# Kernel tuning notes

Hardware: AMD Instinct MI355X
Metric: run time of the kernel (lower is better)

Reference implementation:

```python
import jax, jax.numpy as jnp
import numpy as np

FFT_LEN = 512
FFT_BINS = FFT_LEN // 2 + 1  # 257


def _dft_kernels(fft_len):
    n = np.arange(fft_len)
    k = np.arange(fft_len // 2 + 1).reshape(-1, 1)
    ang = 2.0 * np.pi * k * n / fft_len
    real_kernel = jnp.asarray(np.cos(ang), dtype=jnp.float32)   # (bins, fft_len)
    imag_kernel = jnp.asarray(-np.sin(ang), dtype=jnp.float32)  # (bins, fft_len)
    return real_kernel, imag_kernel


def setup_inputs() -> dict:
    key = jax.random.key(0)
    x = jax.random.normal(key, (16, 4000, FFT_LEN), dtype=jnp.float32)
    real_kernel, imag_kernel = _dft_kernels(FFT_LEN)
    return {"x": x, "real_kernel": real_kernel, "imag_kernel": imag_kernel}


def reference(x, real_kernel, imag_kernel):
    # x: (B, F, N); kernels: (K, N) with K = N//2 + 1
    B, F, _ = x.shape
    real = jnp.einsum("bfn,kn->bfk", x, real_kernel)  # (B, F, K)
    imag = jnp.einsum("bfn,kn->bfk", x, imag_kernel)  # (B, F, K)
    # interleave real/imag per frequency bin: [..., r0, i0, r1, i1, ...]
    out = jnp.stack([real, imag], axis=-1).reshape(B, F, -1)  # (B, F, 2K)
    return out
```

## Files before the change

### kernel.cpp

```cpp
#include <hip/hip_runtime.h>

typedef _Float16 f16x8 __attribute__((ext_vector_type(8)));
typedef float f32x4 __attribute__((ext_vector_type(4)));

#define MDIM 64000
#define KDIM 512
#define NCOLS 514
#define NPAD 640
#define BM 128
#define BN 128
#define BK 64
#define NT 5
#define NWG 2500

#define GLOAD_LDS16(g, l)                                        \
  __builtin_amdgcn_global_load_lds(                              \
      (const __attribute__((address_space(1))) void*)(g),        \
      (__attribute__((address_space(3))) void*)(l), 16, 0, 0)

__global__ void prep_w(const float* __restrict__ rk, const float* __restrict__ ik,
                       _Float16* __restrict__ wb) {
  int n = blockIdx.x;
  int k = threadIdx.x;
  float v = 0.0f;
  if (n < NCOLS) {
    int bin = n >> 1;
    const float* src = (n & 1) ? ik : rk;
    v = src[bin * KDIM + k];
  }
  wb[(size_t)n * KDIM + k] = (_Float16)v;
}

__global__ __launch_bounds__(256, 3)
void dft_gemm(const float* __restrict__ x, const _Float16* __restrict__ wb,
              float* __restrict__ out) {
  __shared__ float As[BM * BK];
  __shared__ _Float16 Bs[BN * BK];

  const int tid = threadIdx.x;
  const int l   = tid & 63;
  const int w   = tid >> 6;
  const int lr  = l & 15;
  const int lg  = l >> 4;
  const int wm  = (w >> 1) * 64;
  const int wn  = (w & 1) * 64;

  const int xcd = blockIdx.x & 7;
  const int lid = blockIdx.x >> 3;
  const int q   = NWG >> 3;
  const int r   = NWG & 7;
  const int wgid = (xcd < r) ? xcd * (q + 1) + lid
                             : r * (q + 1) + (xcd - r) * q + lid;
  const int mt = wgid / NT;
  const int nt = wgid - mt * NT;
  const int m0 = mt * BM;
  const int n0 = nt * BN;

  f32x4 acc[4][4] = {};

  const int arl = l >> 4;
  const int acp = l & 15;
  const int brl = l >> 3;
  const int bcp = l & 7;

  for (int kt = 0; kt < KDIM / BK; ++kt) {
    if (kt) __syncthreads();

#pragma unroll
    for (int s = 0; s < 8; ++s) {
      int r0  = w * 32 + s * 4;
      int row = r0 + arl;
      int cl  = acp ^ (row & 7);
      const float* g = x + (size_t)(m0 + row) * KDIM + kt * BK + cl * 4;
      GLOAD_LDS16(g, &As[r0 * BK]);
    }
#pragma unroll
    for (int s = 0; s < 4; ++s) {
      int r0  = w * 32 + s * 8;
      int row = r0 + brl;
      int cl  = bcp ^ (row & 7);
      const _Float16* g = wb + (size_t)(n0 + row) * KDIM + kt * BK + cl * 8;
      GLOAD_LDS16(g, &Bs[r0 * BK]);
    }
    __syncthreads();

#pragma unroll
    for (int ks = 0; ks < 2; ++ks) {
      f16x8 av[4], bv[4];
#pragma unroll
      for (int fm = 0; fm < 4; ++fm) {
        int row = wm + fm * 16 + lr;
        int c0  = ks * 8 + lg * 2;
        int sw  = row & 7;
        f32x4 lo = *reinterpret_cast<const f32x4*>(&As[row * BK + ((c0 ^ sw) << 2)]);
        f32x4 hi = *reinterpret_cast<const f32x4*>(&As[row * BK + (((c0 + 1) ^ sw) << 2)]);
        f16x8 h;
        h[0] = (_Float16)lo[0]; h[1] = (_Float16)lo[1];
        h[2] = (_Float16)lo[2]; h[3] = (_Float16)lo[3];
        h[4] = (_Float16)hi[0]; h[5] = (_Float16)hi[1];
        h[6] = (_Float16)hi[2]; h[7] = (_Float16)hi[3];
        av[fm] = h;
      }
#pragma unroll
      for (int fn = 0; fn < 4; ++fn) {
        int row = wn + fn * 16 + lr;
        int c   = (ks * 4 + lg) ^ (row & 7);
        bv[fn] = *reinterpret_cast<const f16x8*>(&Bs[row * BK + (c << 3)]);
      }
#pragma unroll
      for (int fm = 0; fm < 4; ++fm)
#pragma unroll
        for (int fn = 0; fn < 4; ++fn)
          acc[fm][fn] = __builtin_amdgcn_mfma_f32_16x16x32_f16(
              av[fm], bv[fn], acc[fm][fn], 0, 0, 0);
    }
  }

#pragma unroll
  for (int fm = 0; fm < 4; ++fm) {
#pragma unroll
    for (int rr = 0; rr < 4; ++rr) {
      int row = m0 + wm + fm * 16 + lg * 4 + rr;
      size_t base = (size_t)row * NCOLS;
#pragma unroll
      for (int fn = 0; fn < 4; ++fn) {
        int col = n0 + wn + fn * 16 + lr;
        if (col < NCOLS) out[base + col] = acc[fm][fn][rr];
      }
    }
  }
}

extern "C" void kernel_launch(void* const* d_in, const int* in_sizes, int n_in,
                              void* d_out, int out_size, void* d_ws, size_t ws_size,
                              hipStream_t stream) {
  const float* x  = (const float*)d_in[0];
  const float* rk = (const float*)d_in[1];
  const float* ik = (const float*)d_in[2];
  float* out = (float*)d_out;
  _Float16* wb = (_Float16*)d_ws;

  prep_w<<<dim3(NPAD), dim3(KDIM), 0, stream>>>(rk, ik, wb);

  dim3 grid(NWG);
  dft_gemm<<<grid, dim3(256), 0, stream>>>(x, wb, out);
}
```

Baseline: 81.90 us.

## Double-buffer LDS and convert A to fp16 via registers before staging

Loads of the fp32 input tile now go through registers. They are converted to fp16 once and stored into a swizzled fp16 LDS buffer, replacing the earlier direct global-to-LDS fp32 copy that was converted on every LDS read. A and B are double-buffered, so the loads for the next K tile are issued before computing on the current one, and only one barrier is needed per iteration. This trades extra VGPRs for prefetched A data (launch bounds lowered from 3 to 2 waves per SIMD) for overlap of memory and MFMA work and halved A LDS traffic.

```diff
diff --git a/kernel.cpp b/kernel.cpp
--- a/kernel.cpp
+++ b/kernel.cpp
@@ -10,6 +10,7 @@
 #define BM 128
 #define BN 128
 #define BK 64
+#define KT (KDIM / BK)
 #define NT 5
 #define NWG 2500
 
@@ -31,11 +32,11 @@
   wb[(size_t)n * KDIM + k] = (_Float16)v;
 }
 
-__global__ __launch_bounds__(256, 3)
+__global__ __launch_bounds__(256, 2)
 void dft_gemm(const float* __restrict__ x, const _Float16* __restrict__ wb,
               float* __restrict__ out) {
-  __shared__ float As[BM * BK];
-  __shared__ _Float16 Bs[BN * BK];
+  __shared__ _Float16 As[2][BM * BK];
+  __shared__ _Float16 Bs[2][BN * BK];
 
   const int tid = threadIdx.x;
   const int l   = tid & 63;
@@ -58,62 +59,93 @@
 
   f32x4 acc[4][4] = {};
 
-  const int arl = l >> 4;
-  const int acp = l & 15;
+  const int arow = tid >> 1;
+  const int acol = (tid & 1) * 32;
+  const float* aptr = x + (size_t)(m0 + arow) * KDIM + acol;
+
   const int brl = l >> 3;
   const int bcp = l & 7;
 
-  for (int kt = 0; kt < KDIM / BK; ++kt) {
-    if (kt) __syncthreads();
+  f32x4 areg[8];
 
-#pragma unroll
-    for (int s = 0; s < 8; ++s) {
-      int r0  = w * 32 + s * 4;
-      int row = r0 + arl;
-      int cl  = acp ^ (row & 7);
-      const float* g = x + (size_t)(m0 + row) * KDIM + kt * BK + cl * 4;
-      GLOAD_LDS16(g, &As[r0 * BK]);
+#define ISSUE_A(t)                                                        \
+  {                                                                       \
+    _Pragma("unroll")                                                     \
+    for (int j = 0; j < 8; ++j)                                           \
+      areg[j] = *reinterpret_cast<const f32x4*>(aptr + (t) * BK + j * 4); \
+  }
+
+#define WRITE_A(buf)                                                      \
+  {                                                                       \
+    _Pragma("unroll")                                                     \
+    for (int c = 0; c < 4; ++c) {                                         \
+      f16x8 h;                                                            \
+      _Pragma("unroll")                                                   \
+      for (int e = 0; e < 4; ++e) {                                       \
+        h[e]     = (_Float16)areg[c * 2][e];                              \
+        h[e + 4] = (_Float16)areg[c * 2 + 1][e];                          \
+      }                                                                   \
+      int pc = ((tid & 1) * 4 + c) ^ (arow & 7);                          \
+      *reinterpret_cast<f16x8*>(&As[buf][arow * BK + pc * 8]) = h;        \
+    }                                                                     \
+  }
+
+#define ISSUE_B(t, buf)                                                   \
+  {                                                                       \
+    _Pragma("unroll")                                                     \
+    for (int s = 0; s < 4; ++s) {                                         \
+      int r0  = w * 32 + s * 8;                                           \
+      int row = r0 + brl;                                                 \
+      int cl  = bcp ^ (row & 7);                                          \
+      const _Float16* g =                                                 \
+          wb + (size_t)(n0 + row) * KDIM + (t) * BK + cl * 8;             \
+      GLOAD_LDS16(g, &Bs[buf][r0 * BK]);                                  \
+    }                                                                     \
+  }
+
+#define COMPUTE(buf)                                                      \
+  {                                                                       \
+    _Pragma("unroll")                                                     \
+    for (int ks = 0; ks < 2; ++ks) {                                      \
+      f16x8 av[4], bv[4];                                                 \
+      _Pragma("unroll")                                                   \
+      for (int fm = 0; fm < 4; ++fm) {                                    \
+        int row = wm + fm * 16 + lr;                                      \
+        int c   = (ks * 4 + lg) ^ (row & 7);                              \
+        av[fm] = *reinterpret_cast<const f16x8*>(&As[buf][row * BK + c * 8]); \
+      }                                                                   \
+      _Pragma("unroll")                                                   \
+      for (int fn = 0; fn < 4; ++fn) {                                    \
+        int row = wn + fn * 16 + lr;                                      \
+        int c   = (ks * 4 + lg) ^ (row & 7);                              \
+        bv[fn] = *reinterpret_cast<const f16x8*>(&Bs[buf][row * BK + c * 8]); \
+      }                                                                   \
+      _Pragma("unroll")                                                   \
+      for (int fm = 0; fm < 4; ++fm)                                      \
+        _Pragma("unroll")                                                 \
+        for (int fn = 0; fn < 4; ++fn)                                    \
+          acc[fm][fn] = __builtin_amdgcn_mfma_f32_16x16x32_f16(           \
+              av[fm], bv[fn], acc[fm][fn], 0, 0, 0);                      \
+    }                                                                     \
+  }
+
+  ISSUE_B(0, 0);
+  ISSUE_A(0);
+  WRITE_A(0);
+  __syncthreads();
+
+  int cur = 0;
+  for (int t = 0; t < KT; ++t) {
+    if (t + 1 < KT) {
+      ISSUE_B(t + 1, cur ^ 1);
+      ISSUE_A(t + 1);
     }
-#pragma unroll
-    for (int s = 0; s < 4; ++s) {
-      int r0  = w * 32 + s * 8;
-      int row = r0 + brl;
-      int cl  = bcp ^ (row & 7);
-      const _Float16* g = wb + (size_t)(n0 + row) * KDIM + kt * BK + cl * 8;
-      GLOAD_LDS16(g, &Bs[r0 * BK]);
+    COMPUTE(cur);
+    if (t + 1 < KT) {
+      WRITE_A(cur ^ 1);
+      __syncthreads();
     }
-    __syncthreads();
-
-#pragma unroll
-    for (int ks = 0; ks < 2; ++ks) {
-      f16x8 av[4], bv[4];
-#pragma unroll
-      for (int fm = 0; fm < 4; ++fm) {
-        int row = wm + fm * 16 + lr;
-        int c0  = ks * 8 + lg * 2;
-        int sw  = row & 7;
-        f32x4 lo = *reinterpret_cast<const f32x4*>(&As[row * BK + ((c0 ^ sw) << 2)]);
-        f32x4 hi = *reinterpret_cast<const f32x4*>(&As[row * BK + (((c0 + 1) ^ sw) << 2)]);
-        f16x8 h;
-        h[0] = (_Float16)lo[0]; h[1] = (_Float16)lo[1];
-        h[2] = (_Float16)lo[2]; h[3] = (_Float16)lo[3];
-        h[4] = (_Float16)hi[0]; h[5] = (_Float16)hi[1];
-        h[6] = (_Float16)hi[2]; h[7] = (_Float16)hi[3];
-        av[fm] = h;
-      }
-#pragma unroll
-      for (int fn = 0; fn < 4; ++fn) {
-        int row = wn + fn * 16 + lr;
-        int c   = (ks * 4 + lg) ^ (row & 7);
-        bv[fn] = *reinterpret_cast<const f16x8*>(&Bs[row * BK + (c << 3)]);
-      }
-#pragma unroll
-      for (int fm = 0; fm < 4; ++fm)
-#pragma unroll
-        for (int fn = 0; fn < 4; ++fn)
-          acc[fm][fn] = __builtin_amdgcn_mfma_f32_16x16x32_f16(
-              av[fm], bv[fn], acc[fm][fn], 0, 0, 0);
-    }
+    cur ^= 1;
   }
 
 #pragma unroll
@@ -129,6 +161,10 @@
       }
     }
   }
+#undef ISSUE_A
+#undef WRITE_A
+#undef ISSUE_B
+#undef COMPUTE
 }
 
 extern "C" void kernel_launch(void* const* d_in, const int* in_sizes, int n_in,
```

After: 122.2 us. +49.2%, slower.

## Drop padded fifth N-tile; compute Nyquist bin as alternating sum in-kernel

Applied to the files above, without the earlier changes.

The output has 514 columns, which previously needed a fifth, mostly-padding 128-wide N tile. Now only 512 columns go through the MFMA GEMM. The Nyquist bin (real part = alternating-sign sum of x, imaginary part = 0) is computed from the A tile already in LDS by the nt==0 workgroups and written separately. This removes 20% of the workgroups and the wasted MFMA work. In exchange the nt==0 blocks do extra LDS reads each k-step, and the Nyquist value uses an fp32 sum while the other bins go through fp16 inputs.

```diff
diff --git a/kernel.cpp b/kernel.cpp
--- a/kernel.cpp
+++ b/kernel.cpp
@@ -6,12 +6,13 @@
 #define MDIM 64000
 #define KDIM 512
 #define NCOLS 514
-#define NPAD 640
+#define NPAD 512
 #define BM 128
 #define BN 128
 #define BK 64
-#define NT 5
-#define NWG 2500
+#define KT (KDIM / BK)
+#define NT 4
+#define NWG 2000
 
 #define GLOAD_LDS16(g, l)                                        \
   __builtin_amdgcn_global_load_lds(                              \
@@ -22,13 +23,9 @@
                        _Float16* __restrict__ wb) {
   int n = blockIdx.x;
   int k = threadIdx.x;
-  float v = 0.0f;
-  if (n < NCOLS) {
-    int bin = n >> 1;
-    const float* src = (n & 1) ? ik : rk;
-    v = src[bin * KDIM + k];
-  }
-  wb[(size_t)n * KDIM + k] = (_Float16)v;
+  int bin = n >> 1;
+  const float* src = (n & 1) ? ik : rk;
+  wb[(size_t)n * KDIM + k] = (_Float16)src[bin * KDIM + k];
 }
 
 __global__ __launch_bounds__(256, 3)
@@ -45,25 +42,21 @@
   const int wm  = (w >> 1) * 64;
   const int wn  = (w & 1) * 64;
 
-  const int xcd = blockIdx.x & 7;
-  const int lid = blockIdx.x >> 3;
-  const int q   = NWG >> 3;
-  const int r   = NWG & 7;
-  const int wgid = (xcd < r) ? xcd * (q + 1) + lid
-                             : r * (q + 1) + (xcd - r) * q + lid;
-  const int mt = wgid / NT;
-  const int nt = wgid - mt * NT;
+  const int wgid = (blockIdx.x & 7) * (NWG / 8) + (blockIdx.x >> 3);
+  const int mt = wgid >> 2;
+  const int nt = wgid & 3;
   const int m0 = mt * BM;
   const int n0 = nt * BN;
 
   f32x4 acc[4][4] = {};
+  float nyq = 0.0f;
 
   const int arl = l >> 4;
   const int acp = l & 15;
   const int brl = l >> 3;
   const int bcp = l & 7;
 
-  for (int kt = 0; kt < KDIM / BK; ++kt) {
+  for (int kt = 0; kt < KT; ++kt) {
     if (kt) __syncthreads();
 
 #pragma unroll
@@ -114,6 +107,17 @@
           acc[fm][fn] = __builtin_amdgcn_mfma_f32_16x16x32_f16(
               av[fm], bv[fn], acc[fm][fn], 0, 0, 0);
     }
+
+    if (nt == 0) {
+      const int nrow = tid >> 1;
+      const int half = tid & 1;
+#pragma unroll
+      for (int j = 0; j < 8; ++j) {
+        int c = (half * 8 + j) ^ (nrow & 7);
+        f32x4 v = *reinterpret_cast<const f32x4*>(&As[nrow * BK + (c << 2)]);
+        nyq += (v[0] - v[1]) + (v[2] - v[3]);
+      }
+    }
   }
 
 #pragma unroll
@@ -123,10 +127,17 @@
       int row = m0 + wm + fm * 16 + lg * 4 + rr;
       size_t base = (size_t)row * NCOLS;
 #pragma unroll
-      for (int fn = 0; fn < 4; ++fn) {
-        int col = n0 + wn + fn * 16 + lr;
-        if (col < NCOLS) out[base + col] = acc[fm][fn][rr];
-      }
+      for (int fn = 0; fn < 4; ++fn)
+        out[base + n0 + wn + fn * 16 + lr] = acc[fm][fn][rr];
+    }
+  }
+
+  if (nt == 0) {
+    float tot = nyq + __shfl_xor(nyq, 1);
+    if ((tid & 1) == 0) {
+      size_t base = (size_t)(m0 + (tid >> 1)) * NCOLS;
+      out[base + 512] = tot;
+      out[base + 513] = 0.0f;
     }
   }
 }
```

Result: faster. 80.11 us, median of 2 (-2.2%).
